# Optimization experiments

Measured on AMD Instinct MI355X. Metric: run time of the kernel, lower is better.

Reference implementation:

```python
import jax, jax.numpy as jnp
import numpy as np

B, T, D, H, O = 128, 2048, 128, 1024, 32
LAST = 20          # last_n_outputs
ALPHA = 0.9        # leak rate
SPARSITY = 0.8


def _make_w_r(rng):
    # Faithful to torch __init__: randn, /max, sparsify, /spectral radius
    w_r = rng.standard_normal((H, H))
    w_r = w_r / np.max(w_r)
    w_r = np.where(rng.random(w_r.shape) < SPARSITY, 0.0, w_r)
    max_abs_eig = np.max(np.abs(np.linalg.eigvals(w_r)))
    return (w_r / max_abs_eig).astype(np.float32)


def setup_inputs() -> dict:
    key = jax.random.key(0)
    k_x, k_in, k_w, k_b = jax.random.split(key, 4)
    rng = np.random.default_rng(0)
    x = jax.random.normal(k_x, (B, T, D), dtype=jnp.float32)
    w_in = jax.random.normal(k_in, (D, H), dtype=jnp.float32) * 0.2
    w_r = jnp.asarray(_make_w_r(rng))
    W = jax.random.normal(k_w, (H * LAST, O), dtype=jnp.float32) * 0.02
    b = jax.random.normal(k_b, (O,), dtype=jnp.float32) * 0.02
    return {"x": x, "w_in": w_in, "w_r": w_r, "W": W, "b": b}


def reference(x, w_in, w_r, W, b):
    # Precompute the non-recurrent term in one batched GEMM: [B,T,H]
    xw = jnp.einsum('btd,dh->bth', x, w_in)

    # t == 0: h0 = 0, and original code sets h = h_hat (no leaky mix)
    h = jnp.tanh(xw[:, 0])  # [B, H]

    def step(h, xt):
        h_hat = jnp.tanh(xt + h @ w_r)
        return (1.0 - ALPHA) * h + ALPHA * h_hat, None

    # steps 1 .. T-LAST-1 : no outputs collected
    xw_mid = jnp.swapaxes(xw[:, 1:T - LAST], 0, 1)   # [T-LAST-1, B, H]
    h, _ = jax.lax.scan(step, h, xw_mid)

    def step_out(h, xt):
        h_hat = jnp.tanh(xt + h @ w_r)
        h_new = (1.0 - ALPHA) * h + ALPHA * h_hat
        return h_new, h_new

    # last LAST steps: collect hidden states
    xw_tail = jnp.swapaxes(xw[:, T - LAST:], 0, 1)   # [LAST, B, H]
    _, hs = jax.lax.scan(step_out, h, xw_tail)       # [LAST, B, H]

    # concat in time order along feature dim -> [B, LAST*H]
    out_cat = jnp.transpose(hs, (1, 0, 2)).reshape(B, LAST * H)
    return out_cat @ W + b
```

## Files before the change

kernel.cpp:

```cpp
#include <hip/hip_runtime.h>
#include <stdint.h>
#include <stddef.h>

#define B_    128
#define T_    2048
#define D_    128
#define H_    1024
#define O_    32
#define LAST_ 20

#define NB_   8
#define NC_   16
#define RING_ 4
#define TWARM_ 8

typedef __bf16 bf16x8 __attribute__((ext_vector_type(8)));
typedef __bf16 bf16x4 __attribute__((ext_vector_type(4)));
typedef float  f32x4  __attribute__((ext_vector_type(4)));
typedef unsigned int u32x4 __attribute__((ext_vector_type(4)));

union Pack8  { unsigned long long u;    bf16x4 v; };
union Pack16 { unsigned long long u[2]; u32x4 d; bf16x8 v; };

__device__ __forceinline__ float tanh_fast(float s) {
    float a = fminf(fmaxf(s, -12.0f), 12.0f);
    float e = __expf(2.0f * a);
    return (e - 1.0f) / (e + 1.0f);
}

__global__ __launch_bounds__(256, 1) void esn_persist(
    const float* __restrict__ x, const float* __restrict__ w_in,
    const float* __restrict__ w_r, __bf16* __restrict__ h_exA,
    __bf16* __restrict__ h_exB, float* __restrict__ hs,
    int* __restrict__ flags)
{
    __shared__ bf16x8 ls[2][16][128];

    const int wg  = (int)blockIdx.x;
    const int bb  = wg & (NB_ - 1);
    const int cb  = wg >> 3;
    const int tid = (int)threadIdx.x;
    const int wv  = tid >> 6;
    const int ln  = tid & 63;
    const int nn  = ln & 15;
    const int q   = ln >> 4;
    const int b0  = bb * 16;
    const int n0  = cb * 64 + wv * 16;

    const unsigned long long tdead =
        __builtin_amdgcn_s_memrealtime() + 300000000ull;

    int xcc;
    asm volatile("s_getreg_b32 %0, hwreg(HW_REG_XCC_ID)" : "=s"(xcc));
    const int mytag = 0x5A5A0000 | (xcc & 0xFF);
    if (tid == 0)
        __hip_atomic_store(flags + wg, mytag, __ATOMIC_RELAXED,
                           __HIP_MEMORY_SCOPE_AGENT);

    bf16x8 win[4];
    #pragma unroll
    for (int c = 0; c < 4; ++c) {
        bf16x8 f;
        #pragma unroll
        for (int j = 0; j < 8; ++j)
            f[j] = (__bf16)w_in[(size_t)(c * 32 + q * 8 + j) * H_ + (n0 + nn)];
        win[c] = f;
    }
    bf16x8 wr[32];
    #pragma unroll
    for (int kc = 0; kc < 32; ++kc) {
        bf16x8 f;
        #pragma unroll
        for (int j = 0; j < 8; ++j)
            f[j] = (__bf16)w_r[(size_t)(kc * 32 + q * 8 + j) * H_ + (n0 + nn)];
        wr[kc] = f;
    }

    bool votefast;
    {
        int alleq = 0;
        for (;;) {
            int seen = 1; alleq = 1;
            #pragma unroll
            for (int k = 0; k < NC_; ++k) {
                int v = __hip_atomic_load(flags + (bb + 8 * k), __ATOMIC_RELAXED,
                                          __HIP_MEMORY_SCOPE_AGENT);
                seen  &= (int)((v & 0xFFFF0000) == 0x5A5A0000);
                alleq &= (int)(v == mytag);
            }
            if (seen) break;
            __builtin_amdgcn_s_sleep(8);
            if (__builtin_amdgcn_s_memrealtime() > tdead) { alleq = 0; break; }
        }
        votefast = (alleq != 0);
    }

    const float* xrow = x + (size_t)(b0 + nn) * T_ * D_ + q * 8;
    const size_t hrow = (size_t)(b0 + nn) * H_;

    f32x4 xn[8];
    bf16x8 xf[4];
    {
        #pragma unroll
        for (int c = 0; c < 4; ++c) {
            xn[2 * c]     = *(const f32x4*)(xrow + c * 32);
            xn[2 * c + 1] = *(const f32x4*)(xrow + c * 32 + 4);
        }
        #pragma unroll
        for (int c = 0; c < 4; ++c) {
            bf16x8 f;
            #pragma unroll
            for (int j = 0; j < 4; ++j) {
                f[j]     = (__bf16)xn[2 * c][j];
                f[j + 4] = (__bf16)xn[2 * c + 1][j];
            }
            xf[c] = f;
        }
    }

    float hm0 = 0.f, hm1 = 0.f, hm2 = 0.f, hm3 = 0.f;

    for (int t = 0; t < T_; ++t) {
        {
            const int tn = (t + 1 < T_) ? t + 1 : T_ - 1;
            const float* xp = xrow + (size_t)tn * D_;
            #pragma unroll
            for (int c = 0; c < 4; ++c) {
                xn[2 * c]     = *(const f32x4*)(xp + c * 32);
                xn[2 * c + 1] = *(const f32x4*)(xp + c * 32 + 4);
            }
        }

        f32x4 acc[8];
        #pragma unroll
        for (int i = 0; i < 8; ++i) acc[i] = (f32x4){0.f, 0.f, 0.f, 0.f};

        #pragma unroll
        for (int c = 0; c < 4; ++c)
            acc[c] = __builtin_amdgcn_mfma_f32_16x16x32_bf16(win[c], xf[c], acc[c], 0, 0, 0);

        if (t > 0) {
            const unsigned long long want1 =
                (unsigned long long)((((t - 1) >> 2) & 1) ^ 1) * 0x100000001ull;
            const int sb = (t - 1) & 1;
            const size_t slotoff =
                (size_t)((t - 1) & (RING_ - 1)) * (B_ * H_) + (size_t)b0 * H_;
            Pack16 pk[8];
            bool have = false;

            if (votefast && t >= TWARM_) {
                const __bf16* hbase = h_exA + slotoff;
                int budget = 512;
                for (;;) {
                    #pragma unroll
                    for (int i = 0; i < 8; ++i) {
                        const int p = wv * 512 + i * 64 + ln;
                        const __bf16* gp = hbase + (size_t)(p >> 7) * H_ + (p & 127) * 8;
                        asm volatile("global_load_dwordx4 %0, %1, off sc0 nt"
                                     : "=v"(pk[i].d) : "v"(gp) : "memory");
                    }
                    asm volatile("s_waitcnt vmcnt(0)"
                                 : "+v"(pk[0].d), "+v"(pk[1].d), "+v"(pk[2].d),
                                   "+v"(pk[3].d), "+v"(pk[4].d), "+v"(pk[5].d),
                                   "+v"(pk[6].d), "+v"(pk[7].d) :: "memory");
                    __builtin_amdgcn_sched_barrier(0);
                    unsigned ok = 1u;
                    #pragma unroll
                    for (int i = 0; i < 8; ++i) {
                        ok &= (unsigned)(((pk[i].u[0] ^ want1) & 0x100000001ull) == 0);
                        ok &= (unsigned)(((pk[i].u[1] ^ want1) & 0x100000001ull) == 0);
                    }
                    if (__all(ok != 0u)) { have = true; break; }
                    if (--budget == 0) break;
                }
            }

            if (!have) {
                const __bf16* hbase = h_exB + slotoff;
                int spins = 0;
                for (;;) {
                    #pragma unroll
                    for (int i = 0; i < 8; ++i) {
                        const int p = wv * 512 + i * 64 + ln;
                        const unsigned long long* gp = (const unsigned long long*)
                            (hbase + (size_t)(p >> 7) * H_ + (p & 127) * 8);
                        pk[i].u[0] = __hip_atomic_load(gp, __ATOMIC_RELAXED,
                                                       __HIP_MEMORY_SCOPE_AGENT);
                        pk[i].u[1] = __hip_atomic_load(gp + 1, __ATOMIC_RELAXED,
                                                       __HIP_MEMORY_SCOPE_AGENT);
                    }
                    unsigned ok = 1u;
                    #pragma unroll
                    for (int i = 0; i < 8; ++i) {
                        ok &= (unsigned)(((pk[i].u[0] ^ want1) & 0x100000001ull) == 0);
                        ok &= (unsigned)(((pk[i].u[1] ^ want1) & 0x100000001ull) == 0);
                    }
                    if (__all(ok != 0u)) break;
                    __builtin_amdgcn_s_sleep(1);
                    if (((++spins) & 63) == 0 &&
                        __builtin_amdgcn_s_memrealtime() > tdead) break;
                }
            }

            #pragma unroll
            for (int i = 0; i < 8; ++i) {
                const int p = wv * 512 + i * 64 + ln;
                const int r = p >> 7, ch = p & 127;
                ls[sb][r][ch ^ (r & 7)] = pk[i].v;
            }

            __syncthreads();

            #pragma unroll
            for (int kc = 0; kc < 32; ++kc) {
                bf16x8 a = ls[sb][nn][(kc * 4 + q) ^ (nn & 7)];
                acc[kc & 7] = __builtin_amdgcn_mfma_f32_16x16x32_bf16(wr[kc], a, acc[kc & 7], 0, 0, 0);
            }
        }

        const f32x4 asum = ((acc[0] + acc[4]) + (acc[1] + acc[5]))
                         + ((acc[2] + acc[6]) + (acc[3] + acc[7]));
        const float th0 = tanh_fast(asum[0]);
        const float th1 = tanh_fast(asum[1]);
        const float th2 = tanh_fast(asum[2]);
        const float th3 = tanh_fast(asum[3]);
        if (t == 0) {
            hm0 = th0; hm1 = th1; hm2 = th2; hm3 = th3;
        } else {
            hm0 = 0.1f * hm0 + 0.9f * th0;
            hm1 = 0.1f * hm1 + 0.9f * th1;
            hm2 = 0.1f * hm2 + 0.9f * th2;
            hm3 = 0.1f * hm3 + 0.9f * th3;
        }

        {
            Pack8 p;
            p.v = (bf16x4){(__bf16)hm0, (__bf16)hm1, (__bf16)hm2, (__bf16)hm3};
            const unsigned long long tg =
                (unsigned long long)(((t >> 2) & 1) ^ 1) * 0x100000001ull;
            p.u = (p.u & ~0x100000001ull) | tg;
            const size_t poff = (size_t)(t & (RING_ - 1)) * (B_ * H_)
                                + hrow + n0 + q * 4;
            if (votefast) {
                unsigned long long* opA = (unsigned long long*)(h_exA + poff);
                asm volatile("global_store_dwordx2 %0, %1, off sc0"
                             :: "v"(opA), "v"(p.u) : "memory");
            }
            unsigned long long* opB = (unsigned long long*)(h_exB + poff);
            __hip_atomic_store(opB, p.u, __ATOMIC_RELAXED,
                               __HIP_MEMORY_SCOPE_AGENT);
        }

        if (t >= T_ - LAST_) {
            f32x4* sp = (f32x4*)(hs + (size_t)(t - (T_ - LAST_)) * (B_ * H_)
                                    + hrow + n0 + q * 4);
            *sp = (f32x4){hm0, hm1, hm2, hm3};
        }
        #pragma unroll
        for (int c = 0; c < 4; ++c) {
            bf16x8 f;
            #pragma unroll
            for (int j = 0; j < 4; ++j) {
                f[j]     = (__bf16)xn[2 * c][j];
                f[j + 4] = (__bf16)xn[2 * c + 1][j];
            }
            xf[c] = f;
        }
    }
}

__global__ __launch_bounds__(256) void esn_out(
    const float* __restrict__ hs, const float* __restrict__ Wm,
    const float* __restrict__ bias, float* __restrict__ out)
{
    const int b   = (int)blockIdx.x;
    const int tid = (int)threadIdx.x;
    float acc[O_];
    #pragma unroll
    for (int o = 0; o < O_; ++o) acc[o] = 0.f;

    for (int k = tid; k < LAST_ * H_; k += 256) {
        const float hv = hs[(size_t)(k >> 10) * (B_ * H_) + (size_t)b * H_ + (k & (H_ - 1))];
        const f32x4* wp = (const f32x4*)(Wm + (size_t)k * O_);
        #pragma unroll
        for (int v = 0; v < 8; ++v) {
            f32x4 w4 = wp[v];
            acc[4 * v + 0] = fmaf(hv, w4[0], acc[4 * v + 0]);
            acc[4 * v + 1] = fmaf(hv, w4[1], acc[4 * v + 1]);
            acc[4 * v + 2] = fmaf(hv, w4[2], acc[4 * v + 2]);
            acc[4 * v + 3] = fmaf(hv, w4[3], acc[4 * v + 3]);
        }
    }

    __shared__ float red[256][O_ + 1];
    #pragma unroll
    for (int o = 0; o < O_; ++o) red[tid][o] = acc[o];
    __syncthreads();
    if (tid < O_) {
        float s = bias[tid];
        for (int i = 0; i < 256; ++i) s += red[i][tid];
        out[(size_t)b * O_ + tid] = s;
    }
}

extern "C" void kernel_launch(void* const* d_in, const int* in_sizes, int n_in,
                              void* d_out, int out_size, void* d_ws, size_t ws_size,
                              hipStream_t stream)
{
    const float* x    = (const float*)d_in[0];
    const float* w_in = (const float*)d_in[1];
    const float* w_r  = (const float*)d_in[2];
    const float* Wm   = (const float*)d_in[3];
    const float* bias = (const float*)d_in[4];
    float* out        = (float*)d_out;

    const size_t flag_bytes = 4096;
    const size_t ring_bytes = (size_t)RING_ * B_ * H_ * sizeof(__bf16);
    const size_t hs_bytes   = (size_t)LAST_ * B_ * H_ * sizeof(float);
    if (ws_size < flag_bytes + 2 * ring_bytes + hs_bytes) return;

    int*    flags = (int*)d_ws;
    __bf16* h_exA = (__bf16*)((char*)d_ws + flag_bytes);
    __bf16* h_exB = (__bf16*)((char*)d_ws + flag_bytes + ring_bytes);
    float*  hs    = (float*)((char*)d_ws + flag_bytes + 2 * ring_bytes);

    hipMemsetAsync(flags, 0x00, flag_bytes, stream);
    hipMemsetAsync(h_exA, 0xAA, 2 * ring_bytes, stream);

    hipLaunchKernelGGL(esn_persist, dim3(NB_ * NC_), dim3(256), 0, stream,
                       x, w_in, w_r, h_exA, h_exB, hs, flags);
    hipLaunchKernelGGL(esn_out, dim3(B_), dim3(256), 0, stream,
                       hs, Wm, bias, out);
}
```

Measured before the change: 6.650 ms.

## Poll a single sentinel row before bulk h exchange load; drop redundant B-buffer stores

On the fast path, each wave now spins on a small 8-byte sentinel load from the last row of the producer slot until its tag matches. Only then does it issue the full 8x16-byte load of the hidden-state slice, instead of repeatedly reloading the whole slice while polling. The fallback to the atomic B buffer is removed on the fast path; those loops now break only on a timeout. Producers stop writing the B buffer once past the warmup steps when the fast path is active. This cuts polling traffic and store bandwidth, but it relies on the sentinel row being ordered with the other rows and gives up the budgeted fallback path.

Result: faster. 6.197 ms (-6.8%).

```diff
diff --git a/kernel.cpp b/kernel.cpp
--- a/kernel.cpp
+++ b/kernel.cpp
@@ -98,6 +98,8 @@
     const float* xrow = x + (size_t)(b0 + nn) * T_ * D_ + q * 8;
     const size_t hrow = (size_t)(b0 + nn) * H_;
 
+    const int scol = (ln >> 2) * 64 + (ln & 3) * 16 + 12;
+
     f32x4 xn[8];
     bf16x8 xf[4];
     {
@@ -146,36 +148,50 @@
             const size_t slotoff =
                 (size_t)((t - 1) & (RING_ - 1)) * (B_ * H_) + (size_t)b0 * H_;
             Pack16 pk[8];
-            bool have = false;
 
             if (votefast && t >= TWARM_) {
-                const __bf16* hbase = h_exA + slotoff;
-                int budget = 512;
-                for (;;) {
-                    #pragma unroll
-                    for (int i = 0; i < 8; ++i) {
-                        const int p = wv * 512 + i * 64 + ln;
-                        const __bf16* gp = hbase + (size_t)(p >> 7) * H_ + (p & 127) * 8;
-                        asm volatile("global_load_dwordx4 %0, %1, off sc0 nt"
-                                     : "=v"(pk[i].d) : "v"(gp) : "memory");
+                {
+                    const unsigned long long* sp = (const unsigned long long*)
+                        (h_exA + slotoff + 15 * H_ + scol);
+                    int spins = 0;
+                    for (;;) {
+                        unsigned long long s;
+                        asm volatile("global_load_dwordx2 %0, %1, off sc0 nt"
+                                     : "=v"(s) : "v"(sp) : "memory");
+                        asm volatile("s_waitcnt vmcnt(0)" : "+v"(s) :: "memory");
+                        if (__all(((s ^ want1) & 0x100000001ull) == 0)) break;
+                        if (((++spins) & 255) == 0 &&
+                            __builtin_amdgcn_s_memrealtime() > tdead) break;
                     }
-                    asm volatile("s_waitcnt vmcnt(0)"
-                                 : "+v"(pk[0].d), "+v"(pk[1].d), "+v"(pk[2].d),
-                                   "+v"(pk[3].d), "+v"(pk[4].d), "+v"(pk[5].d),
-                                   "+v"(pk[6].d), "+v"(pk[7].d) :: "memory");
-                    __builtin_amdgcn_sched_barrier(0);
-                    unsigned ok = 1u;
-                    #pragma unroll
-                    for (int i = 0; i < 8; ++i) {
-                        ok &= (unsigned)(((pk[i].u[0] ^ want1) & 0x100000001ull) == 0);
-                        ok &= (unsigned)(((pk[i].u[1] ^ want1) & 0x100000001ull) == 0);
+                }
+                {
+                    int spins = 0;
+                    for (;;) {
+                        #pragma unroll
+                        for (int i = 0; i < 8; ++i) {
+                            const int p = wv * 512 + i * 64 + ln;
+                            const __bf16* gp = h_exA + slotoff
+                                + (size_t)(p >> 7) * H_ + (p & 127) * 8;
+                            asm volatile("global_load_dwordx4 %0, %1, off sc0 nt"
+                                         : "=v"(pk[i].d) : "v"(gp) : "memory");
+                        }
+                        asm volatile("s_waitcnt vmcnt(0)"
+                                     : "+v"(pk[0].d), "+v"(pk[1].d), "+v"(pk[2].d),
+                                       "+v"(pk[3].d), "+v"(pk[4].d), "+v"(pk[5].d),
+                                       "+v"(pk[6].d), "+v"(pk[7].d) :: "memory");
+                        __builtin_amdgcn_sched_barrier(0);
+                        unsigned ok = 1u;
+                        #pragma unroll
+                        for (int i = 0; i < 8; ++i) {
+                            ok &= (unsigned)(((pk[i].u[0] ^ want1) & 0x100000001ull) == 0);
+                            ok &= (unsigned)(((pk[i].u[1] ^ want1) & 0x100000001ull) == 0);
+                        }
+                        if (__all(ok != 0u)) break;
+                        if (((++spins) & 63) == 0 &&
+                            __builtin_amdgcn_s_memrealtime() > tdead) break;
                     }
-                    if (__all(ok != 0u)) { have = true; break; }
-                    if (--budget == 0) break;
                 }
-            }
-
-            if (!have) {
+            } else {
                 const __bf16* hbase = h_exB + slotoff;
                 int spins = 0;
                 for (;;) {
@@ -245,10 +261,16 @@
                 unsigned long long* opA = (unsigned long long*)(h_exA + poff);
                 asm volatile("global_store_dwordx2 %0, %1, off sc0"
                              :: "v"(opA), "v"(p.u) : "memory");
-            }
-            unsigned long long* opB = (unsigned long long*)(h_exB + poff);
-            __hip_atomic_store(opB, p.u, __ATOMIC_RELAXED,
-                               __HIP_MEMORY_SCOPE_AGENT);
+                if (t < TWARM_) {
+                    unsigned long long* opB = (unsigned long long*)(h_exB + poff);
+                    __hip_atomic_store(opB, p.u, __ATOMIC_RELAXED,
+                                       __HIP_MEMORY_SCOPE_AGENT);
+                }
+            } else {
+                unsigned long long* opB = (unsigned long long*)(h_exB + poff);
+                __hip_atomic_store(opB, p.u, __ATOMIC_RELAXED,
+                                   __HIP_MEMORY_SCOPE_AGENT);
+            }
         }
 
         if (t >= T_ - LAST_) {
```
